# Performance work log

Hardware: AMD Instinct MI355X
Metric: run time of the kernel (lower is better)

Reference implementation:

```python
import jax, jax.numpy as jnp
import numpy as np
from jax import lax

B, CIN, HID, H, W, PS = 16, 64, 64, 128, 128, 8
PH, PW = H // PS, W // PS          # patch grid (16,16)
N = PH * PW                        # 256 patch tokens


def setup_inputs() -> dict:
    key = jax.random.key(0)
    ks = jax.random.split(key, 16)

    def wn(k, shape, s=0.02):
        return jax.random.normal(k, shape, jnp.float32) * s

    z = lambda n: jnp.zeros((n,), jnp.float32)
    return {
        "x": jax.random.normal(ks[0], (B, CIN, H, W), jnp.float32),
        "c": jax.random.normal(ks[1], (B, HID, H, W), jnp.float32),
        "h": jax.random.normal(ks[2], (B, HID, H, W), jnp.float32),
        "m": jax.random.normal(ks[3], (B, HID, H, W), jnp.float32),
        "conv_w": wn(ks[4], (4 * HID, CIN + HID, 3, 3)), "conv_b": z(4 * HID),
        "gn_w": jnp.ones((4 * HID,), jnp.float32), "gn_b": z(4 * HID),
        "qh_w": wn(ks[5], (HID, HID)), "qh_b": z(HID),
        "kh_w": wn(ks[6], (HID, HID)), "kh_b": z(HID),
        "vh_w": wn(ks[7], (HID, HID)), "vh_b": z(HID),
        "km_w": wn(ks[8], (HID, HID)), "km_b": z(HID),
        "vm_w": wn(ks[9], (HID, HID)), "vm_b": z(HID),
        "z_w": wn(ks[10], (2 * HID, 2 * HID)), "z_b": z(2 * HID),
        "m_w": wn(ks[11], (3 * HID, 3 * HID)), "m_b": z(3 * HID),
    }


def _conv1x1(t, w, b):
    return jnp.einsum('bchw,oc->bohw', t, w) + b[None, :, None, None]


def _pool(t):
    # Faithful to torch: view(B,C,N,-1).mean(-1) on row-major flattened HW
    b, c = t.shape[:2]
    return t.reshape(b, c, N, -1).mean(-1)  # (B,C,N)


def _cell(x, c, h, m, conv_w, conv_b, gn_w, gn_b,
          qh_w, qh_b, kh_w, kh_b, vh_w, vh_b, km_w, km_b, vm_w, vm_b,
          z_w, z_b, m_w, m_b):
    # --- ConvLSTM gating: 3x3 conv + GroupNorm(groups == channels) ---
    comb = jnp.concatenate([x, h], axis=1)
    cc = lax.conv_general_dilated(comb, conv_w, (1, 1), 'SAME',
                                  dimension_numbers=('NCHW', 'OIHW', 'NCHW'))
    cc = cc + conv_b[None, :, None, None]
    mu = cc.mean((2, 3), keepdims=True)
    var = cc.var((2, 3), keepdims=True)
    cc = (cc - mu) * lax.rsqrt(var + 1e-5)
    cc = cc * gn_w[None, :, None, None] + gn_b[None, :, None, None]
    i, f, g, o = jnp.split(cc, 4, axis=1)
    c_next = jax.nn.sigmoid(f) * c + jax.nn.sigmoid(i) * jnp.tanh(g)
    h_next = jax.nn.sigmoid(o) * jnp.tanh(c_next)

    # --- SA memory module ---
    Kp = _pool(_conv1x1(h_next, kh_w, kh_b))          # (B,C,N)
    Qp = _pool(_conv1x1(h_next, qh_w, qh_b))          # (B,C,N)
    Vp = _pool(_conv1x1(h_next, vh_w, vh_b))          # (B,C,N)
    Kmp = _pool(_conv1x1(m, km_w, km_b))
    Vmp = _pool(_conv1x1(m, vm_w, vm_b))

    A_h = jax.nn.softmax(jnp.einsum('bcn,bcm->bnm', Qp, Kp), axis=-1)   # (B,N,N)
    A_m = jax.nn.softmax(jnp.einsum('bcn,bcm->bnm', Qp, Kmp), axis=-1)
    Zh = jnp.einsum('bnm,bcm->bcn', A_h, Vp).reshape(-1, HID, PH, PW)
    Zm = jnp.einsum('bnm,bcm->bcn', A_m, Vmp).reshape(-1, HID, PH, PW)

    # bilinear upsample (half-pixel centers == torch align_corners=False)
    Zh = jax.image.resize(Zh, (Zh.shape[0], HID, H, W), 'bilinear')
    Zm = jax.image.resize(Zm, (Zm.shape[0], HID, H, W), 'bilinear')

    Z = _conv1x1(jnp.concatenate([Zh, Zm], axis=1), z_w, z_b)
    combined = _conv1x1(jnp.concatenate([Z, h_next], axis=1), m_w, m_b)
    mo, mg, mi = jnp.split(combined, 3, axis=1)
    mi = jax.nn.sigmoid(mi)
    new_m = (1 - mi) * m + mi * jnp.tanh(mg)
    new_h = jax.nn.sigmoid(mo) * new_m
    return new_h, c_next, new_m


def reference(x, c, h, m, conv_w, conv_b, gn_w, gn_b,
              qh_w, qh_b, kh_w, kh_b, vh_w, vh_b, km_w, km_b, vm_w, vm_b,
              z_w, z_b, m_w, m_b):
    return _cell(x, c, h, m, conv_w, conv_b, gn_w, gn_b,
                 qh_w, qh_b, kh_w, kh_b, vh_w, vh_b, km_w, km_b, vm_w, vm_b,
                 z_w, z_b, m_w, m_b)
```

## Files before the change

kernel.cpp:

```cpp
#include <hip/hip_runtime.h>
#include <hip/hip_bf16.h>
#include <math.h>

typedef __attribute__((ext_vector_type(4))) float f4;
typedef __attribute__((ext_vector_type(4))) float f32x4;
typedef __attribute__((ext_vector_type(8))) short bf16x8;

#define HSZ 128
#define WSZ 128
#define HW 16384

__device__ __forceinline__ float sigm(float x){ return 1.f/(1.f+__expf(-x)); }
__device__ __forceinline__ float tanh_fast(float x){ return 1.f - 2.f/(1.f+__expf(2.f*x)); }
__device__ __forceinline__ float bf_lo(unsigned u){ return __uint_as_float(u<<16); }
__device__ __forceinline__ float bf_hi(unsigned u){ return __uint_as_float(u & 0xffff0000u); }

__global__ void k_setup(const float* __restrict__ conv_w, const float* __restrict__ m_w,
                        __hip_bfloat16* __restrict__ wB, __hip_bfloat16* __restrict__ WhB){
  int idx = blockIdx.x*256 + threadIdx.x;
  if (idx < 294912){
    int kk = idx & 31;
    int oc = (idx>>5) & 255;
    int q  = idx >> 13;
    int dx = q % 3; int t2 = q / 3; int ck = t2 & 3; int dy = t2 >> 2;
    int ic = ck*32 + kk;
    wB[idx] = __float2bfloat16(conv_w[((oc*128+ic)*3+dy)*3+dx]);
  } else if (idx < 294912 + 12288){
    int j = idx - 294912;
    int o = j >> 6, ci = j & 63;
    WhB[j] = __float2bfloat16(m_w[o*192 + 128 + ci]);
  }
}

__global__ void k_w2(const float* __restrict__ m_w, const float* __restrict__ z_w,
                     const float* __restrict__ z_b, const float* __restrict__ m_b,
                     float* __restrict__ W2, float* __restrict__ bc){
  int idx = blockIdx.x*256 + threadIdx.x;
  if (idx < 24576){
    int o = idx >> 7, zi = idx & 127;
    float s = 0.f;
    for (int zo=0; zo<128; zo++) s += m_w[o*192+zo]*z_w[zo*128+zi];
    W2[idx] = s;
  } else if (idx < 24576 + 192){
    int o = idx - 24576;
    float s = m_b[o];
    for (int zo=0; zo<128; zo++) s += m_w[o*192+zo]*z_b[zo];
    bc[o] = s;
  }
}

__global__ __launch_bounds__(256) void k_im(const float* __restrict__ x,
    const float* __restrict__ h, __hip_bfloat16* __restrict__ im, int b0){
  __shared__ __hip_bfloat16 T[128*136];
  int bid = blockIdx.x; int y = bid & 127, bl = bid >> 7; int b = b0 + bl;
  int t = threadIdx.x;
  for (int idx=t; idx<4096; idx+=256){
    int c = idx>>5, xq = idx&31;
    const float* src = (c<64)? x : h; int cm = c&63;
    f4 v = *(const f4*)(src + ((((size_t)b*64+cm)*HSZ + y)*WSZ + xq*4));
    #pragma unroll
    for (int j=0;j<4;j++) T[(xq*4+j)*136 + c] = __float2bfloat16(v[j]);
  }
  __syncthreads();
  for (int idx=t; idx<2048; idx+=256){
    int xx = idx>>4, q = idx&15;
    uint4 v = *(const uint4*)&T[xx*136 + q*8];
    *(uint4*)(im + ((((size_t)bl*HSZ + y)*WSZ + xx)*128 + q*8)) = v;
  }
}

__global__ __launch_bounds__(256) void k_conv(const __hip_bfloat16* __restrict__ im,
    const __hip_bfloat16* __restrict__ wB, __hip_bfloat16* __restrict__ cc, int b0){
  __shared__ __align__(16) short LDS[17408];
  short* buf0 = LDS;
  short* buf1 = LDS + 5280;
  int bid = blockIdx.x;
  int y = bid & 127, bl = bid >> 7; int b = b0 + bl;
  int oc0 = blockIdx.y * 128;
  int t = threadIdx.x;
  int lane = t & 63, w = t >> 6;
  int ln15 = lane & 15, h8 = (lane>>4)*8;
  int ocw = (w>>1)*64, pxw = (w&1)*64;
  int px0 = t>>2, q0 = t&3;

  f32x4 acc[4][4];
  #pragma unroll
  for (int mi=0;mi<4;mi++)
    #pragma unroll
    for (int ni=0;ni<4;ni++) acc[mi][ni] = (f32x4){0.f,0.f,0.f,0.f};

  auto stage = [&](int s, short* dst){
    int dy = s>>2, ck = s&3;
    int yy = y + dy - 1;
    bool yok = (yy>=0) && (yy<HSZ);
    const __hip_bfloat16* rb = im + (((size_t)bl*HSZ + yy)*WSZ)*128 + ck*32;
    uint4 v0 = make_uint4(0u,0u,0u,0u);
    uint4 v1 = make_uint4(0u,0u,0u,0u);
    uint4 v2 = make_uint4(0u,0u,0u,0u);
    if (yok && px0>=1)       v0 = *(const uint4*)(rb + (size_t)(px0-1)*128 + q0*8);
    if (yok)                 v1 = *(const uint4*)(rb + (size_t)(px0+63)*128 + q0*8);
    if (yok && t<4)          v2 = *(const uint4*)(rb + (size_t)127*128 + q0*8);
    *(uint4*)&dst[px0*40 + q0*8]      = v0;
    *(uint4*)&dst[(px0+64)*40 + q0*8] = v1;
    if (t<16) *(uint4*)&dst[(128+(t>>2))*40 + q0*8] = v2;
  };
  auto compute = [&](int s, const short* src){
    #pragma unroll
    for (int dx=0; dx<3; dx++){
      const __hip_bfloat16* wp = wB + (((size_t)(s*3+dx)*256 + oc0 + ocw + ln15)*32 + h8);
      bf16x8 af[4], bfr[4];
      #pragma unroll
      for (int i=0;i<4;i++) af[i]  = *(const bf16x8*)(wp + (size_t)i*16*32);
      #pragma unroll
      for (int i=0;i<4;i++) bfr[i] = *(const bf16x8*)&src[(pxw + i*16 + ln15 + dx)*40 + h8];
      #pragma unroll
      for (int mi=0;mi<4;mi++)
        #pragma unroll
        for (int ni=0;ni<4;ni++)
          acc[mi][ni] = __builtin_amdgcn_mfma_f32_16x16x32_bf16(af[mi], bfr[ni], acc[mi][ni], 0, 0, 0);
    }
  };

  stage(0, buf0);
  __syncthreads();
  for (int s=0; s<12; s++){
    short* cur = (s&1)? buf1 : buf0;
    short* nxt = (s&1)? buf0 : buf1;
    if (s < 11) stage(s+1, nxt);
    compute(s, cur);
    __syncthreads();
  }

  __hip_bfloat16* OutL = (__hip_bfloat16*)LDS;
  int hv4 = (lane>>4)*4;
  #pragma unroll
  for (int mi=0;mi<4;mi++)
    #pragma unroll
    for (int ni=0;ni<4;ni++){
      #pragma unroll
      for (int r=0;r<4;r++)
        OutL[(ocw + mi*16 + hv4 + r)*136 + pxw + ni*16 + ln15] = __float2bfloat16(acc[mi][ni][r]);
    }
  __syncthreads();
  for (int idx=t; idx<2048; idx+=256){
    int oc = idx>>4, qc = idx&15;
    uint4 v = *(const uint4*)&OutL[oc*136 + qc*8];
    *(uint4*)(cc + ((((size_t)b*256 + oc0 + oc)*HSZ + y)*WSZ + qc*8)) = v;
  }
}

__global__ __launch_bounds__(256) void k_gnstats(const __hip_bfloat16* __restrict__ cc,
    const float* __restrict__ gn_w, const float* __restrict__ gn_b,
    float* __restrict__ scale, float* __restrict__ shift){
  int bc_ = blockIdx.x;
  const uint4* p = (const uint4*)(cc + (size_t)bc_*HW);
  float s=0.f, ss=0.f;
  for (int ch=threadIdx.x; ch<2048; ch+=256){
    uint4 u = p[ch];
    unsigned uw[4] = {u.x, u.y, u.z, u.w};
    #pragma unroll
    for (int w=0; w<4; w++){
      float a = bf_lo(uw[w]);
      float b2 = bf_hi(uw[w]);
      s += a + b2; ss += a*a + b2*b2;
    }
  }
  for (int off=1; off<64; off<<=1){ s += __shfl_xor(s, off); ss += __shfl_xor(ss, off); }
  __shared__ float rs_[4], rss_[4];
  int wv = threadIdx.x>>6, ln = threadIdx.x&63;
  if (ln==0){ rs_[wv]=s; rss_[wv]=ss; }
  __syncthreads();
  if (threadIdx.x==0){
    float S = rs_[0]+rs_[1]+rs_[2]+rs_[3];
    float SS = rss_[0]+rss_[1]+rss_[2]+rss_[3];
    float mu = S*(1.f/16384.f);
    float var = SS*(1.f/16384.f) - mu*mu;
    float r = rsqrtf(var + 1e-5f);
    int oc = bc_ & 255;
    float sc = gn_w[oc]*r;
    scale[bc_] = sc;
    shift[bc_] = gn_b[oc] - mu*sc;
  }
}

__global__ __launch_bounds__(256) void k_gate(const __hip_bfloat16* __restrict__ cc,
    const float* __restrict__ cin, const float* __restrict__ scale, const float* __restrict__ shift,
    float* __restrict__ out_c, float* __restrict__ out_h, float* __restrict__ poolh){
  int bid = blockIdx.x;
  int b = bid>>6, c = bid&63;
  size_t base_i = ((size_t)b*256 + c)*HW;
  const uint4* pi = (const uint4*)(cc + base_i);
  const uint4* pf = (const uint4*)(cc + base_i + (size_t)64*HW);
  const uint4* pg = (const uint4*)(cc + base_i + (size_t)128*HW);
  const uint4* po = (const uint4*)(cc + base_i + (size_t)192*HW);
  float ssi = scale[b*256+c],     shi = shift[b*256+c];
  float ssf = scale[b*256+64+c],  shf = shift[b*256+64+c];
  float ssg = scale[b*256+128+c], shg = shift[b*256+128+c];
  float sso = scale[b*256+192+c], sho = shift[b*256+192+c];
  size_t pbase = ((size_t)b*64 + c)*HW;
  const f4* pc_ = (const f4*)(cin + pbase);
  f4* oc_ = (f4*)(out_c + pbase);
  f4* oh_ = (f4*)(out_h + pbase);
  int lane = threadIdx.x & 63;
  for (int ch = threadIdx.x; ch < 2048; ch += 256){
    uint4 ui = pi[ch], uf = pf[ch], ug = pg[ch], uo = po[ch];
    unsigned iu[4]={ui.x,ui.y,ui.z,ui.w}, fu[4]={uf.x,uf.y,uf.z,uf.w};
    unsigned gu[4]={ug.x,ug.y,ug.z,ug.w}, ou[4]={uo.x,uo.y,uo.z,uo.w};
    f4 ca = pc_[ch*2], cb = pc_[ch*2+1];
    float cvv[8] = {ca[0],ca[1],ca[2],ca[3],cb[0],cb[1],cb[2],cb[3]};
    float rc[8], rh[8];
    #pragma unroll
    for (int w=0; w<4; w++){
      #pragma unroll
      for (int hl=0; hl<2; hl++){
        int k = w*2+hl;
        float iv = (hl? bf_hi(iu[w]) : bf_lo(iu[w]))*ssi + shi;
        float fv = (hl? bf_hi(fu[w]) : bf_lo(fu[w]))*ssf + shf;
        float gv = (hl? bf_hi(gu[w]) : bf_lo(gu[w]))*ssg + shg;
        float ov = (hl? bf_hi(ou[w]) : bf_lo(ou[w]))*sso + sho;
        float cn = sigm(fv)*cvv[k] + sigm(iv)*tanh_fast(gv);
        rc[k] = cn;
        rh[k] = sigm(ov)*tanh_fast(cn);
      }
    }
    f4 o0 = {rc[0],rc[1],rc[2],rc[3]}, o1 = {rc[4],rc[5],rc[6],rc[7]};
    f4 h0 = {rh[0],rh[1],rh[2],rh[3]}, h1 = {rh[4],rh[5],rh[6],rh[7]};
    oc_[ch*2] = o0; oc_[ch*2+1] = o1;
    oh_[ch*2] = h0; oh_[ch*2+1] = h1;
    float ps = ((rh[0]+rh[1])+(rh[2]+rh[3])) + ((rh[4]+rh[5])+(rh[6]+rh[7]));
    ps += __shfl_xor(ps, 1);
    ps += __shfl_xor(ps, 2);
    ps += __shfl_xor(ps, 4);
    if ((lane & 7) == 0) poolh[(size_t)bid*256 + (ch>>3)] = ps*(1.f/64.f);
  }
}

__global__ __launch_bounds__(256) void k_poolm(const float* __restrict__ m_in,
    float* __restrict__ poolm){
  int pc = blockIdx.x;
  const float* src = m_in + (size_t)pc*HW;
  float* dst = poolm + (size_t)pc*256;
  int n = threadIdx.x;
  const f4* p = (const f4*)(src + n*64);
  float s = 0.f;
  #pragma unroll
  for (int i=0;i<16;i++){ f4 v = p[i]; s += (v[0]+v[1]) + (v[2]+v[3]); }
  dst[n] = s*(1.f/64.f);
}

__global__ __launch_bounds__(256) void k_proj(const float* __restrict__ pool,
    const float* qw,const float* qb,const float* kw,const float* kb,
    const float* vw,const float* vb,const float* kmw,const float* kmb,
    const float* vmw,const float* vmb, float* __restrict__ proj){
  int bid = blockIdx.x;
  int p = bid % 5, b = bid / 5;
  const float* P = pool + (p>=3? 262144:0) + (size_t)b*16384;
  const float* W; const float* Bs;
  if (p==0){W=qw;Bs=qb;} else if(p==1){W=kw;Bs=kb;} else if(p==2){W=vw;Bs=vb;}
  else if (p==3){W=kmw;Bs=kmb;} else {W=vmw;Bs=vmb;}
  int n = threadIdx.x;
  float acc[64];
  #pragma unroll
  for (int o=0;o<64;o++) acc[o]=0.f;
  for (int c=0;c<64;c++){
    float pv = P[c*256+n];
    #pragma unroll
    for (int o=0;o<64;o++) acc[o] += W[o*64+c]*pv;
  }
  float* dst = proj + (size_t)p*262144 + (size_t)b*16384;
  #pragma unroll
  for (int o=0;o<64;o++) dst[o*256+n] = acc[o] + Bs[o];
}

__global__ __launch_bounds__(256) void k_scores(const float* __restrict__ proj, float* __restrict__ A){
  int n = blockIdx.x, ty = blockIdx.y, b = blockIdx.z;
  const float* Q = proj + (size_t)b*16384;
  const float* K = proj + (size_t)(ty==0?1:3)*262144 + (size_t)b*16384;
  int mm = threadIdx.x;
  float s = 0.f;
  for (int c=0;c<64;c++) s += Q[c*256+n]*K[c*256+mm];
  float mx = s;
  for (int off=1; off<64; off<<=1) mx = fmaxf(mx, __shfl_xor(mx, off));
  __shared__ float r1[4], r2[4];
  int wv = threadIdx.x>>6, ln = threadIdx.x&63;
  if (ln==0) r1[wv]=mx;
  __syncthreads();
  mx = fmaxf(fmaxf(r1[0],r1[1]),fmaxf(r1[2],r1[3]));
  float e = __expf(s-mx);
  float sm = e;
  for (int off=1; off<64; off<<=1) sm += __shfl_xor(sm, off);
  if (ln==0) r2[wv]=sm;
  __syncthreads();
  sm = r2[0]+r2[1]+r2[2]+r2[3];
  A[(((size_t)ty*16+b)*256+n)*256+mm] = e/sm;
}

__global__ __launch_bounds__(256) void k_apply(const float* __restrict__ proj,
    const float* __restrict__ A, float* __restrict__ Zcat){
  int ty = blockIdx.x, b = blockIdx.y, cq = blockIdx.z;
  const float* V = proj + (size_t)(ty==0?2:4)*262144 + (size_t)b*16384 + (size_t)cq*16*256;
  const float* Ar = A + (((size_t)ty*16+b)*256 + threadIdx.x)*256;
  float acc[16];
  #pragma unroll
  for (int c=0;c<16;c++) acc[c]=0.f;
  for (int mm=0; mm<256; mm++){
    float a = Ar[mm];
    #pragma unroll
    for (int c=0;c<16;c++) acc[c] += V[c*256+mm]*a;
  }
  float* dst = Zcat + ((size_t)b*128 + ty*64 + cq*16)*256 + threadIdx.x;
  #pragma unroll
  for (int c=0;c<16;c++) dst[c*256] = acc[c];
}

__global__ __launch_bounds__(256) void k_csmall(const float* __restrict__ Zcat,
    const float* __restrict__ W2, float* __restrict__ Cs){
  int oq = blockIdx.x, b = blockIdx.y;
  int o0 = oq*32;
  int n = threadIdx.x;
  float acc[32];
  #pragma unroll
  for (int o=0;o<32;o++) acc[o]=0.f;
  for (int zi=0; zi<128; zi++){
    float z = Zcat[((size_t)b*128+zi)*256 + n];
    #pragma unroll
    for (int o=0;o<32;o++) acc[o] += W2[(o0+o)*128 + zi]*z;
  }
  float* dst = Cs + ((size_t)b*192 + o0)*256 + n;
  #pragma unroll
  for (int o=0;o<32;o++) dst[o*256] = acc[o];
}

__global__ __launch_bounds__(256, 3) void k_final(
    const float* __restrict__ hn, const float* __restrict__ m_in,
    const __hip_bfloat16* __restrict__ WhB, const float* __restrict__ Cs,
    const float* __restrict__ bcv, float* __restrict__ out_h, float* __restrict__ out_m){
  __shared__ float rowF[64*69];
  __shared__ float CsL[192*36];
  int bid = blockIdx.x;
  int xh = bid & 1, y = (bid>>1) & 127, b = bid >> 8;
  int x0 = xh*64;
  int t = threadIdx.x, lane = t & 63, w = t >> 6;
  int ln15 = lane & 15, hi = lane >> 4, h8 = hi*8;

  float sy = (y+0.5f)*0.125f - 0.5f;
  int iy = (int)floorf(sy); float fy = sy - (float)iy;
  int ya = min(max(iy,0),15), yb = min(max(iy+1,0),15);

  for (int idx=t; idx<1024; idx+=256){
    int c = idx>>4, xq = idx&15;
    f4 v = *(const f4*)(hn + ((((size_t)b*64+c)*HSZ + y)*WSZ + x0 + xq*4));
    float* d = &rowF[c*69 + xq*4];
    d[0]=v[0]; d[1]=v[1]; d[2]=v[2]; d[3]=v[3];
  }
  for (int idx=t; idx<1536; idx+=256){
    int cp = idx>>3, rr = (idx>>2)&1, q = idx&3;
    int ry = rr? yb : ya;
    f4 v = *(const f4*)(Cs + (((size_t)b*192 + cp)*256 + ry*16 + q*4));
    *(f4*)&CsL[cp*36 + rr*16 + q*4] = v;
  }
  __syncthreads();

  bf16x8 bfr[2];
  #pragma unroll
  for (int ks=0; ks<2; ks++){
    union { bf16x8 v; __hip_bfloat16 e[8]; } u;
    #pragma unroll
    for (int j=0;j<8;j++)
      u.e[j] = __float2bfloat16(rowF[(ks*32 + h8 + j)*69 + w*16 + ln15]);
    bfr[ks] = u.v;
  }
  f32x4 acc[12];
  #pragma unroll
  for (int mt=0;mt<12;mt++) acc[mt] = (f32x4){0.f,0.f,0.f,0.f};
  #pragma unroll
  for (int ks=0; ks<2; ks++){
    #pragma unroll
    for (int mt=0; mt<12; mt++){
      bf16x8 af = *(const bf16x8*)(WhB + ((mt*16+ln15)*64 + ks*32 + h8));
      acc[mt] = __builtin_amdgcn_mfma_f32_16x16x32_bf16(af, bfr[ks], acc[mt], 0, 0, 0);
    }
  }

  int xg = x0 + w*16 + ln15;
  float sx = (xg+0.5f)*0.125f - 0.5f;
  int ix = (int)floorf(sx); float fx = sx - (float)ix;
  int xa = min(max(ix,0),15), xb2 = min(max(ix+1,0),15);
  float w00=(1.f-fy)*(1.f-fx), w01=(1.f-fy)*fx, w10=fy*(1.f-fx), w11=fy*fx;
  int o00 = xa, o01 = xb2, o10 = 16+xa, o11 = 16+xb2;
  #pragma unroll
  for (int mt=0; mt<4; mt++){
    #pragma unroll
    for (int r=0; r<4; r++){
      int c = mt*16 + hi*4 + r;
      const float* p0 = &CsL[c*36];
      const float* p1 = &CsL[(64+c)*36];
      const float* p2 = &CsL[(128+c)*36];
      float vo = acc[mt][r]   + p0[o00]*w00 + p0[o01]*w01 + p0[o10]*w10 + p0[o11]*w11 + bcv[c];
      float vg = acc[mt+4][r] + p1[o00]*w00 + p1[o01]*w01 + p1[o10]*w10 + p1[o11]*w11 + bcv[64+c];
      float vi = acc[mt+8][r] + p2[o00]*w00 + p2[o01]*w01 + p2[o10]*w10 + p2[o11]*w11 + bcv[128+c];
      size_t pix = (((size_t)b*64+c)*HSZ + y)*WSZ + xg;
      float mv = m_in[pix];
      float smi = sigm(vi);
      float nm = (1.f-smi)*mv + smi*tanh_fast(vg);
      float nh = sigm(vo)*nm;
      out_h[pix] = nh;
      out_m[pix] = nm;
    }
  }
}

extern "C" void kernel_launch(void* const* d_in, const int* in_sizes, int n_in,
                              void* d_out, int out_size, void* d_ws, size_t ws_size,
                              hipStream_t stream){
  (void)in_sizes; (void)n_in; (void)out_size; (void)ws_size;
  const float* x    = (const float*)d_in[0];
  const float* cst  = (const float*)d_in[1];
  const float* h    = (const float*)d_in[2];
  const float* m    = (const float*)d_in[3];
  const float* conv_w = (const float*)d_in[4];
  const float* gn_w = (const float*)d_in[6];
  const float* gn_b = (const float*)d_in[7];
  const float* qh_w = (const float*)d_in[8];  const float* qh_b = (const float*)d_in[9];
  const float* kh_w = (const float*)d_in[10]; const float* kh_b = (const float*)d_in[11];
  const float* vh_w = (const float*)d_in[12]; const float* vh_b = (const float*)d_in[13];
  const float* km_w = (const float*)d_in[14]; const float* km_b = (const float*)d_in[15];
  const float* vm_w = (const float*)d_in[16]; const float* vm_b = (const float*)d_in[17];
  const float* z_w  = (const float*)d_in[18]; const float* z_b  = (const float*)d_in[19];
  const float* m_w  = (const float*)d_in[20]; const float* m_b  = (const float*)d_in[21];

  float* out   = (float*)d_out;
  float* out_h = out;
  float* out_c = out + 16777216;
  float* out_m = out + 33554432;

  char* ws = (char*)d_ws;
  __hip_bfloat16* cc = (__hip_bfloat16*)ws;
  float* proj = (float*)(ws + 2097152);
  float* Amat = (float*)(ws + 7340032);
  float* Zcat = (float*)(ws + 15728640);
  float* Cs   = (float*)(ws + 17825792);
  __hip_bfloat16* im = (__hip_bfloat16*)(ws + 134217728);
  float* pool = (float*)(ws + 134217728);
  __hip_bfloat16* wB = (__hip_bfloat16*)(ws + 150994944);
  __hip_bfloat16* WhB = (__hip_bfloat16*)(ws + 151584768);
  float* W2   = (float*)(ws + 151633920);
  float* bcv  = (float*)(ws + 151732224);
  float* gnsc = (float*)(ws + 151732992);
  float* gnsh = (float*)(ws + 151749376);

  hipLaunchKernelGGL(k_setup, dim3(1200), dim3(256), 0, stream, conv_w, m_w, wB, WhB);
  hipLaunchKernelGGL(k_w2, dim3(97), dim3(256), 0, stream, m_w, z_w, z_b, m_b, W2, bcv);
  for (int q = 0; q < 4; q++){
    hipLaunchKernelGGL(k_im,   dim3(512),    dim3(256), 0, stream, x, h, im, q*4);
    hipLaunchKernelGGL(k_conv, dim3(512, 2), dim3(256), 0, stream, im, wB, cc, q*4);
  }
  hipLaunchKernelGGL(k_gnstats, dim3(4096), dim3(256), 0, stream, cc, gn_w, gn_b, gnsc, gnsh);
  hipLaunchKernelGGL(k_gate, dim3(1024), dim3(256), 0, stream, cc, cst, gnsc, gnsh, out_c, out_h, pool);
  hipLaunchKernelGGL(k_poolm, dim3(1024), dim3(256), 0, stream, m, pool + 262144);
  hipLaunchKernelGGL(k_proj, dim3(80), dim3(256), 0, stream, pool,
                     qh_w,qh_b,kh_w,kh_b,vh_w,vh_b,km_w,km_b,vm_w,vm_b, proj);
  hipLaunchKernelGGL(k_scores, dim3(256,2,16), dim3(256), 0, stream, proj, Amat);
  hipLaunchKernelGGL(k_apply, dim3(2,16,4), dim3(256), 0, stream, proj, Amat, Zcat);
  hipLaunchKernelGGL(k_csmall, dim3(6,16), dim3(256), 0, stream, Zcat, W2, Cs);
  hipLaunchKernelGGL(k_final, dim3(4096), dim3(256), 0, stream, out_h, m, WhB, Cs, bcv, out_h, out_m);
}
```

Baseline: 664.8 us.

## Fuse GroupNorm statistics into conv epilogue via atomics and remap conv block order

The separate GroupNorm statistics kernel, which re-read the whole bf16 conv output, is removed. The conv kernel's store loop now computes per-channel partial sums and sums of squares, reduces them across 16 lanes, and atomically accumulates them into zeroed buffers. A tiny finalize kernel then turns those sums into scale and shift. The conv block index is also permuted so that consecutive blocks are spread across rows and batches, which may change cache or XCD locality, and the atomics add contention and make float summation order nondeterministic.

```diff
diff --git a/kernel.cpp b/kernel.cpp
--- a/kernel.cpp
+++ b/kernel.cpp
@@ -70,11 +70,13 @@
 }
 
 __global__ __launch_bounds__(256) void k_conv(const __hip_bfloat16* __restrict__ im,
-    const __hip_bfloat16* __restrict__ wB, __hip_bfloat16* __restrict__ cc, int b0){
+    const __hip_bfloat16* __restrict__ wB, __hip_bfloat16* __restrict__ cc, int b0,
+    float* __restrict__ gs, float* __restrict__ gss){
   __shared__ __align__(16) short LDS[17408];
   short* buf0 = LDS;
   short* buf1 = LDS + 5280;
-  int bid = blockIdx.x;
+  int bid0 = blockIdx.x;
+  int bid = (bid0 & 7)*64 + (bid0 >> 3);
   int y = bid & 127, bl = bid >> 7; int b = b0 + bl;
   int oc0 = blockIdx.y * 128;
   int t = threadIdx.x;
@@ -146,41 +148,33 @@
     int oc = idx>>4, qc = idx&15;
     uint4 v = *(const uint4*)&OutL[oc*136 + qc*8];
     *(uint4*)(cc + ((((size_t)b*256 + oc0 + oc)*HSZ + y)*WSZ + qc*8)) = v;
-  }
-}
-
-__global__ __launch_bounds__(256) void k_gnstats(const __hip_bfloat16* __restrict__ cc,
-    const float* __restrict__ gn_w, const float* __restrict__ gn_b,
-    float* __restrict__ scale, float* __restrict__ shift){
-  int bc_ = blockIdx.x;
-  const uint4* p = (const uint4*)(cc + (size_t)bc_*HW);
-  float s=0.f, ss=0.f;
-  for (int ch=threadIdx.x; ch<2048; ch+=256){
-    uint4 u = p[ch];
-    unsigned uw[4] = {u.x, u.y, u.z, u.w};
-    #pragma unroll
-    for (int w=0; w<4; w++){
-      float a = bf_lo(uw[w]);
-      float b2 = bf_hi(uw[w]);
-      s += a + b2; ss += a*a + b2*b2;
-    }
-  }
-  for (int off=1; off<64; off<<=1){ s += __shfl_xor(s, off); ss += __shfl_xor(ss, off); }
-  __shared__ float rs_[4], rss_[4];
-  int wv = threadIdx.x>>6, ln = threadIdx.x&63;
-  if (ln==0){ rs_[wv]=s; rss_[wv]=ss; }
-  __syncthreads();
-  if (threadIdx.x==0){
-    float S = rs_[0]+rs_[1]+rs_[2]+rs_[3];
-    float SS = rss_[0]+rss_[1]+rss_[2]+rss_[3];
-    float mu = S*(1.f/16384.f);
-    float var = SS*(1.f/16384.f) - mu*mu;
-    float r = rsqrtf(var + 1e-5f);
-    int oc = bc_ & 255;
-    float sc = gn_w[oc]*r;
-    scale[bc_] = sc;
-    shift[bc_] = gn_b[oc] - mu*sc;
-  }
+    unsigned uw[4] = {v.x, v.y, v.z, v.w};
+    float ls = 0.f, lss = 0.f;
+    #pragma unroll
+    for (int k2=0;k2<4;k2++){
+      float a = bf_lo(uw[k2]), b2 = bf_hi(uw[k2]);
+      ls += a + b2; lss += a*a + b2*b2;
+    }
+    #pragma unroll
+    for (int off=1; off<16; off<<=1){ ls += __shfl_xor(ls, off); lss += __shfl_xor(lss, off); }
+    if ((t & 15) == 0){
+      atomicAdd(&gs [b*256 + oc0 + oc], ls);
+      atomicAdd(&gss[b*256 + oc0 + oc], lss);
+    }
+  }
+}
+
+__global__ void k_gnfin(const float* __restrict__ gn_w, const float* __restrict__ gn_b,
+                        float* __restrict__ gs, float* __restrict__ gss){
+  int i = blockIdx.x*256 + threadIdx.x;
+  float s = gs[i], ss = gss[i];
+  float mu = s*(1.f/16384.f);
+  float var = ss*(1.f/16384.f) - mu*mu;
+  float r = rsqrtf(var + 1e-5f);
+  int oc = i & 255;
+  float sc = gn_w[oc]*r;
+  gs[i]  = sc;
+  gss[i] = gn_b[oc] - mu*sc;
 }
 
 __global__ __launch_bounds__(256) void k_gate(const __hip_bfloat16* __restrict__ cc,
@@ -451,11 +445,12 @@
 
   hipLaunchKernelGGL(k_setup, dim3(1200), dim3(256), 0, stream, conv_w, m_w, wB, WhB);
   hipLaunchKernelGGL(k_w2, dim3(97), dim3(256), 0, stream, m_w, z_w, z_b, m_b, W2, bcv);
+  hipMemsetAsync(gnsc, 0, 32768, stream);
   for (int q = 0; q < 4; q++){
     hipLaunchKernelGGL(k_im,   dim3(512),    dim3(256), 0, stream, x, h, im, q*4);
-    hipLaunchKernelGGL(k_conv, dim3(512, 2), dim3(256), 0, stream, im, wB, cc, q*4);
-  }
-  hipLaunchKernelGGL(k_gnstats, dim3(4096), dim3(256), 0, stream, cc, gn_w, gn_b, gnsc, gnsh);
+    hipLaunchKernelGGL(k_conv, dim3(512, 2), dim3(256), 0, stream, im, wB, cc, q*4, gnsc, gnsh);
+  }
+  hipLaunchKernelGGL(k_gnfin, dim3(16), dim3(256), 0, stream, gn_w, gn_b, gnsc, gnsh);
   hipLaunchKernelGGL(k_gate, dim3(1024), dim3(256), 0, stream, cc, cst, gnsc, gnsh, out_c, out_h, pool);
   hipLaunchKernelGGL(k_poolm, dim3(1024), dim3(256), 0, stream, m, pool + 262144);
   hipLaunchKernelGGL(k_proj, dim3(80), dim3(256), 0, stream, pool,
```

New measurement: 730.9 us. 1.1x slower.
